# Kernel tuning notes

Measured on AMD Instinct MI355X. Metric: run time of the kernel, lower is better.

The kernel has to match this reference:

```python
import jax, jax.numpy as jnp
import numpy as np

NUM_HEADS = 4

def setup_inputs() -> dict:
    key = jax.random.key(0)
    ks = jax.random.split(key, 9)
    C = 256
    def w(k, shape, scale):
        return jax.random.normal(k, shape, dtype=jnp.float32) * scale
    s = 1.0 / np.sqrt(C)
    return {
        'x':  w(ks[0], (1, C, 48, 48), 1.0),
        'Wq': w(ks[1], (C, C), s), 'bq': w(ks[2], (C,), 0.01),
        'Wk': w(ks[3], (C, C), s), 'bk': w(ks[4], (C,), 0.01),
        'Wv': w(ks[5], (C, C), s), 'bv': w(ks[6], (C,), 0.01),
        'Wo': w(ks[7], (C, C), s), 'bo': w(ks[8], (C,), 0.01),
    }

def reference(x, Wq, bq, Wk, bk, Wv, bv, Wo, bo):
    # x: [B, C, H, W] (NCHW like torch). 1x1 convs == per-pixel matmuls in NHWC.
    B, C, H, W = x.shape
    nh = NUM_HEADS
    xt = jnp.transpose(x, (0, 2, 3, 1))                 # [B,H,W,C]
    q = xt @ Wq.T + bq                                  # [B,H,W,Ck]
    k = xt @ Wk.T + bk                                  # [B,H,W,Ck]
    v = xt @ Wv.T + bv                                  # [B,H,W,Cv]
    dk = q.shape[-1] // nh
    dv = v.shape[-1] // nh
    # split heads then FULLY flatten (batch*H*W*heads), as in the original
    qf = q.reshape(B * H * W * nh, dk) / jnp.sqrt(jnp.float32(dk))
    kf = k.reshape(B * H * W * nh, dk)
    vf = v.reshape(B * H * W * nh, dv)
    A = jax.nn.softmax(qf @ kf.T, axis=1)               # [N,N], N = B*H*W*nh
    # dropout is identity in eval mode
    O = A @ vf                                          # [N,dv]
    O = O.reshape(B, H, W, nh * dv)                     # heads folded back into channels
    out = O @ Wo.T + bo                                 # 1x1 output conv
    return jnp.transpose(out, (0, 3, 1, 2))             # [B,Cout,H,W]
```

## Files before the change

### kernel.cpp

```cpp
#include <hip/hip_runtime.h>
#include <stdint.h>

typedef __attribute__((ext_vector_type(4))) float f32x4;
typedef __attribute__((ext_vector_type(8))) short bf16x8;

#define MFMA(a, b, c) __builtin_amdgcn_mfma_f32_16x16x32_bf16(a, b, c, 0, 0, 0)

__device__ __forceinline__ short f2b(float f) {
    uint32_t u = __builtin_bit_cast(uint32_t, f);
    u += 0x7fffu + ((u >> 16) & 1u);
    return (short)(u >> 16);
}

__device__ __forceinline__ float ex2(float x) {
    float r; asm("v_exp_f32 %0, %1" : "=v"(r) : "v"(x)); return r;
}
__device__ __forceinline__ uint32_t cvtpk(float lo, float hi) {
    uint32_t r; asm("v_cvt_pk_bf16_f32 %0, %1, %2" : "=v"(r) : "v"(lo), "v"(hi)); return r;
}
__device__ __forceinline__ float lo2f(uint32_t u) {
    return __builtin_bit_cast(float, (uint32_t)(u << 16));
}
__device__ __forceinline__ float hi2f(uint32_t u) {
    return __builtin_bit_cast(float, (uint32_t)(u & 0xffff0000u));
}

typedef __attribute__((address_space(1))) const uint32_t gu32;
typedef __attribute__((address_space(3))) uint32_t su32;
__device__ __forceinline__ void stage16(const void* g, void* s) {
    __builtin_amdgcn_global_load_lds((gu32*)g, (su32*)s, 16, 0, 0);
}

__device__ __forceinline__ int FSW(int r) { return (r & 3) | (((r >> 3) & 1) << 2); }

#define QSCALE 0.1803368801111601f

__global__ __launch_bounds__(256) void k_prep(
    const float* __restrict__ x,
    const float* __restrict__ Wq, const float* __restrict__ Wk,
    const float* __restrict__ Wv, const float* __restrict__ Wo,
    short* __restrict__ Wall, short* __restrict__ xt) {
    __shared__ float tile[64][65];
    if (blockIdx.x < 1024) {
        int idx = blockIdx.x * 256 + threadIdx.x;
        int row = idx >> 8, col = idx & 255;
        float v;
        if (row < 256)      v = Wq[row * 256 + col];
        else if (row < 512) v = Wk[(row - 256) * 256 + col];
        else if (row < 768) v = Wv[(row - 512) * 256 + col];
        else                v = Wo[(row - 768) * 256 + col];
        Wall[idx] = f2b(v);
    } else {
        int b = blockIdx.x - 1024;
        int pbase = (b % 36) * 64, cbase = (b / 36) * 64;
        int tx = threadIdx.x & 63, tq = threadIdx.x >> 6;
        #pragma unroll
        for (int r = 0; r < 16; r++) {
            int row = tq * 16 + r;
            tile[row][tx] = x[(cbase + row) * 2304 + pbase + tx];
        }
        __syncthreads();
        #pragma unroll
        for (int r = 0; r < 16; r++) {
            int prow = tq * 16 + r;
            xt[(pbase + prow) * 256 + cbase + tx] = f2b(tile[tx][prow]);
        }
    }
}

__global__ __launch_bounds__(256) void k_gemm_qkv(
    const short* __restrict__ Wall, const short* __restrict__ xt,
    const float* __restrict__ bq, const float* __restrict__ bk, const float* __restrict__ bv,
    short* __restrict__ Qf, short* __restrict__ Kf, short* __restrict__ Vt) {
    int t = threadIdx.x, wave = t >> 6, lane = t & 63, lr = lane & 15, lg = lane >> 4;
    int obase = blockIdx.x * 64 + wave * 16;
    int pbase = blockIdx.y * 64;
    const short* arow  = Wall + (obase + lr) * 256 + lg * 8;
    const short* brow0 = xt + (pbase +  0 + lr) * 256 + lg * 8;
    const short* brow1 = xt + (pbase + 16 + lr) * 256 + lg * 8;
    const short* brow2 = xt + (pbase + 32 + lr) * 256 + lg * 8;
    const short* brow3 = xt + (pbase + 48 + lr) * 256 + lg * 8;
    f32x4 acc0 = {0,0,0,0}, acc1 = {0,0,0,0}, acc2 = {0,0,0,0}, acc3 = {0,0,0,0};
    #pragma unroll
    for (int ks = 0; ks < 8; ks++) {
        bf16x8 a = *(const bf16x8*)(arow + ks * 32);
        acc0 = MFMA(a, *(const bf16x8*)(brow0 + ks * 32), acc0);
        acc1 = MFMA(a, *(const bf16x8*)(brow1 + ks * 32), acc1);
        acc2 = MFMA(a, *(const bf16x8*)(brow2 + ks * 32), acc2);
        acc3 = MFMA(a, *(const bf16x8*)(brow3 + ks * 32), acc3);
    }
    int w_idx = obase >> 8;
    const float* bias = (w_idx == 0) ? bq : (w_idx == 1) ? bk : bv;
    f32x4 accs[4] = {acc0, acc1, acc2, acc3};
    #pragma unroll
    for (int i = 0; i < 4; i++) {
        int o = obase + 4 * lg + i;
        int oo = o & 255;
        float b = bias[oo];
        int h = oo >> 6, d = oo & 63;
        #pragma unroll
        for (int ct = 0; ct < 4; ct++) {
            int p = pbase + ct * 16 + lr;
            float val = accs[ct][i] + b;
            int n = p * 4 + h;
            if (w_idx == 0)      Qf[n * 64 + d] = f2b(val * QSCALE);
            else if (w_idx == 1) Kf[n * 64 + d] = f2b(val);
            else                 Vt[d * 9216 + n] = f2b(val);
        }
    }
}

__global__ __launch_bounds__(256) void k_attn(
    const short* __restrict__ Qf, const short* __restrict__ Kf,
    const short* __restrict__ Vt, int keysPer, int ntiles,
    float* __restrict__ ps, uint32_t* __restrict__ pacc) {
    __shared__ short ktile[2][4096];
    __shared__ short vtile[2][4096];
    int t = threadIdx.x, wave = t >> 6, lane = t & 63, lr = lane & 15, lg = lane >> 4;
    int kb = blockIdx.y;
    int qbase = blockIdx.x * 128 + wave * 16;
    int kstart = kb * keysPer;

    const short* qrowA = Qf + (qbase + lr) * 64 + lg * 8;
    bf16x8 qA0 = *(const bf16x8*)(qrowA);
    bf16x8 qA1 = *(const bf16x8*)(qrowA + 32);
    const short* qrowB = qrowA + 64 * 64;
    bf16x8 qB0 = *(const bf16x8*)(qrowB);
    bf16x8 qB1 = *(const bf16x8*)(qrowB + 32);

    bf16x8 ones;
    #pragma unroll
    for (int i = 0; i < 8; i++) ones[i] = (short)0x3F80;

    int sr = lane >> 3, slot = lane & 7;
    int srow0 = wave * 16 + sr, srow1 = srow0 + 8;
    int col0 = (slot ^ FSW(srow0)) << 4;
    int col1 = (slot ^ FSW(srow1)) << 4;
    const char* kS0 = (const char*)Kf + (size_t)(kstart + srow0) * 128 + col0;
    const char* kS1 = (const char*)Kf + (size_t)(kstart + srow1) * 128 + col1;
    const char* vS0 = (const char*)Vt + (size_t)srow0 * 18432 + (size_t)kstart * 2 + col0;
    const char* vS1 = (const char*)Vt + (size_t)srow1 * 18432 + (size_t)kstart * 2 + col1;
    short* kD0[2] = { &ktile[0][wave * 1024], &ktile[1][wave * 1024] };
    short* kD1[2] = { kD0[0] + 512, kD0[1] + 512 };
    short* vD0[2] = { &vtile[0][wave * 1024], &vtile[1][wave * 1024] };
    short* vD1[2] = { vD0[0] + 512, vD0[1] + 512 };

    int perm = (lr & 3) + 8 * (lr >> 2);
    int cb = lg * 16;
    int kOffA0 = perm * 128       + (cb        ^ (FSW(perm) << 4));
    int kOffA1 = perm * 128       + ((cb + 64) ^ (FSW(perm) << 4));
    int kOffB0 = (perm + 4) * 128 + (cb        ^ (FSW(perm + 4) << 4));
    int kOffB1 = (perm + 4) * 128 + ((cb + 64) ^ (FSW(perm + 4) << 4));
    int vOff   = lr * 128         + (cb        ^ (FSW(lr) << 4));

    f32x4 zv = {0,0,0,0};
    f32x4 accA0 = zv, accA1 = zv, accA2 = zv, accA3 = zv, saccA = zv;
    f32x4 accB0 = zv, accB1 = zv, accB2 = zv, accB3 = zv, saccB = zv;

    stage16(kS0, kD0[0]); stage16(kS1, kD1[0]);
    stage16(vS0, vD0[0]); stage16(vS1, vD1[0]);

    for (int tt = 0; tt < ntiles; tt++) {
        __syncthreads();
        int buf = tt & 1;
        if (tt + 1 < ntiles) {
            size_t ko = (size_t)(tt + 1) * 8192, vo = (size_t)(tt + 1) * 128;
            stage16(kS0 + ko, kD0[buf ^ 1]); stage16(kS1 + ko, kD1[buf ^ 1]);
            stage16(vS0 + vo, vD0[buf ^ 1]); stage16(vS1 + vo, vD1[buf ^ 1]);
        }
        const char* kt = (const char*)&ktile[buf][0];
        const char* vt = (const char*)&vtile[buf][0];

        bf16x8 kA0 = *(const bf16x8*)(kt + kOffA0);
        bf16x8 kA1 = *(const bf16x8*)(kt + kOffA1);
        bf16x8 kB0 = *(const bf16x8*)(kt + kOffB0);
        bf16x8 kB1 = *(const bf16x8*)(kt + kOffB1);
        f32x4 sA0 = MFMA(kA0, qA0, zv); sA0 = MFMA(kA1, qA1, sA0);
        f32x4 sA1 = MFMA(kB0, qA0, zv); sA1 = MFMA(kB1, qA1, sA1);
        f32x4 sB0 = MFMA(kA0, qB0, zv); sB0 = MFMA(kA1, qB1, sB0);
        f32x4 sB1 = MFMA(kB0, qB0, zv); sB1 = MFMA(kB1, qB1, sB1);
        kA0 = *(const bf16x8*)(kt + 4096 + kOffA0);
        kA1 = *(const bf16x8*)(kt + 4096 + kOffA1);
        kB0 = *(const bf16x8*)(kt + 4096 + kOffB0);
        kB1 = *(const bf16x8*)(kt + 4096 + kOffB1);
        f32x4 sA2 = MFMA(kA0, qA0, zv); sA2 = MFMA(kA1, qA1, sA2);
        f32x4 sA3 = MFMA(kB0, qA0, zv); sA3 = MFMA(kB1, qA1, sA3);
        f32x4 sB2 = MFMA(kA0, qB0, zv); sB2 = MFMA(kA1, qB1, sB2);
        f32x4 sB3 = MFMA(kB0, qB0, zv); sB3 = MFMA(kB1, qB1, sB3);

        union { uint32_t w[4]; bf16x8 v; } paA, pbA, paB, pbB;
        paA.w[0] = cvtpk(ex2(sA0[0]), ex2(sA0[1]));
        paA.w[1] = cvtpk(ex2(sA0[2]), ex2(sA0[3]));
        paA.w[2] = cvtpk(ex2(sA1[0]), ex2(sA1[1]));
        paA.w[3] = cvtpk(ex2(sA1[2]), ex2(sA1[3]));
        pbA.w[0] = cvtpk(ex2(sA2[0]), ex2(sA2[1]));
        pbA.w[1] = cvtpk(ex2(sA2[2]), ex2(sA2[3]));
        pbA.w[2] = cvtpk(ex2(sA3[0]), ex2(sA3[1]));
        pbA.w[3] = cvtpk(ex2(sA3[2]), ex2(sA3[3]));
        paB.w[0] = cvtpk(ex2(sB0[0]), ex2(sB0[1]));
        paB.w[1] = cvtpk(ex2(sB0[2]), ex2(sB0[3]));
        paB.w[2] = cvtpk(ex2(sB1[0]), ex2(sB1[1]));
        paB.w[3] = cvtpk(ex2(sB1[2]), ex2(sB1[3]));
        pbB.w[0] = cvtpk(ex2(sB2[0]), ex2(sB2[1]));
        pbB.w[1] = cvtpk(ex2(sB2[2]), ex2(sB2[3]));
        pbB.w[2] = cvtpk(ex2(sB3[0]), ex2(sB3[1]));
        pbB.w[3] = cvtpk(ex2(sB3[2]), ex2(sB3[3]));

        bf16x8 v0a = *(const bf16x8*)(vt + vOff);
        bf16x8 v0b = *(const bf16x8*)(vt + (vOff ^ 64));
        bf16x8 v1a = *(const bf16x8*)(vt + vOff + 2048);
        bf16x8 v1b = *(const bf16x8*)(vt + ((vOff + 2048) ^ 64));
        bf16x8 v2a = *(const bf16x8*)(vt + vOff + 4096);
        bf16x8 v2b = *(const bf16x8*)(vt + ((vOff + 4096) ^ 64));
        bf16x8 v3a = *(const bf16x8*)(vt + vOff + 6144);
        bf16x8 v3b = *(const bf16x8*)(vt + ((vOff + 6144) ^ 64));
        accA0 = MFMA(v0a, paA.v, accA0); accA0 = MFMA(v0b, pbA.v, accA0);
        accA1 = MFMA(v1a, paA.v, accA1); accA1 = MFMA(v1b, pbA.v, accA1);
        accA2 = MFMA(v2a, paA.v, accA2); accA2 = MFMA(v2b, pbA.v, accA2);
        accA3 = MFMA(v3a, paA.v, accA3); accA3 = MFMA(v3b, pbA.v, accA3);
        saccA = MFMA(ones, paA.v, saccA); saccA = MFMA(ones, pbA.v, saccA);
        accB0 = MFMA(v0a, paB.v, accB0); accB0 = MFMA(v0b, pbB.v, accB0);
        accB1 = MFMA(v1a, paB.v, accB1); accB1 = MFMA(v1b, pbB.v, accB1);
        accB2 = MFMA(v2a, paB.v, accB2); accB2 = MFMA(v2b, pbB.v, accB2);
        accB3 = MFMA(v3a, paB.v, accB3); accB3 = MFMA(v3b, pbB.v, accB3);
        saccB = MFMA(ones, paB.v, saccB); saccB = MFMA(ones, pbB.v, saccB);
    }

    int gA = blockIdx.x * 8 + wave;
    int gB = gA + 4;
    int pidxA = kb * 576 + gA, pidxB = kb * 576 + gB;
    uint2* outA = (uint2*)pacc + (size_t)pidxA * 256 + lr * 16 + lg;
    uint2* outB = (uint2*)pacc + (size_t)pidxB * 256 + lr * 16 + lg;
    uint2 w;
    w.x = cvtpk(accA0[0], accA0[1]); w.y = cvtpk(accA0[2], accA0[3]); outA[0]  = w;
    w.x = cvtpk(accA1[0], accA1[1]); w.y = cvtpk(accA1[2], accA1[3]); outA[4]  = w;
    w.x = cvtpk(accA2[0], accA2[1]); w.y = cvtpk(accA2[2], accA2[3]); outA[8]  = w;
    w.x = cvtpk(accA3[0], accA3[1]); w.y = cvtpk(accA3[2], accA3[3]); outA[12] = w;
    w.x = cvtpk(accB0[0], accB0[1]); w.y = cvtpk(accB0[2], accB0[3]); outB[0]  = w;
    w.x = cvtpk(accB1[0], accB1[1]); w.y = cvtpk(accB1[2], accB1[3]); outB[4]  = w;
    w.x = cvtpk(accB2[0], accB2[1]); w.y = cvtpk(accB2[2], accB2[3]); outB[8]  = w;
    w.x = cvtpk(accB3[0], accB3[1]); w.y = cvtpk(accB3[2], accB3[3]); outB[12] = w;
    if (lg == 0) {
        ps[pidxA * 16 + lr] = saccA[0];
        ps[pidxB * 16 + lr] = saccB[0];
    }
}

__global__ __launch_bounds__(256) void k_attn_combine(
    const float* __restrict__ ps, const uint32_t* __restrict__ pacc,
    short* __restrict__ Of, int nsplit) {
    int qb = blockIdx.x, t = threadIdx.x;
    int q = t >> 4, dv4 = (t & 15) * 4;
    float S = 0.f;
    f32x4 O = {0, 0, 0, 0};
    for (int s = 0; s < nsplit; s++) {
        S += ps[(s * 576 + qb) * 16 + q];
        uint2 v = ((const uint2*)pacc)[(size_t)(s * 576 + qb) * 256 + t];
        O[0] += lo2f(v.x); O[1] += hi2f(v.x);
        O[2] += lo2f(v.y); O[3] += hi2f(v.y);
    }
    float inv = 1.0f / S;
    uint32_t w0 = cvtpk(O[0] * inv, O[1] * inv);
    uint32_t w1 = cvtpk(O[2] * inv, O[3] * inv);
    int n = qb * 16 + q, p = n >> 2, hh = n & 3;
    uint2 pk; pk.x = w0; pk.y = w1;
    *(uint2*)(&Of[p * 256 + hh * 64 + dv4]) = pk;
}

__global__ __launch_bounds__(256) void k_gemm_out(
    const short* __restrict__ Wo_bf, const short* __restrict__ Of,
    const float* __restrict__ bo, float* __restrict__ out) {
    int t = threadIdx.x, wave = t >> 6, lane = t & 63, lr = lane & 15, lg = lane >> 4;
    int obase = blockIdx.x * 64 + wave * 16;
    int pbase = blockIdx.y * 64;
    const short* arow  = Wo_bf + (obase + lr) * 256 + lg * 8;
    const short* brow0 = Of + (pbase +  0 + lr) * 256 + lg * 8;
    const short* brow1 = Of + (pbase + 16 + lr) * 256 + lg * 8;
    const short* brow2 = Of + (pbase + 32 + lr) * 256 + lg * 8;
    const short* brow3 = Of + (pbase + 48 + lr) * 256 + lg * 8;
    f32x4 acc0 = {0,0,0,0}, acc1 = {0,0,0,0}, acc2 = {0,0,0,0}, acc3 = {0,0,0,0};
    #pragma unroll
    for (int ks = 0; ks < 8; ks++) {
        bf16x8 a = *(const bf16x8*)(arow + ks * 32);
        acc0 = MFMA(a, *(const bf16x8*)(brow0 + ks * 32), acc0);
        acc1 = MFMA(a, *(const bf16x8*)(brow1 + ks * 32), acc1);
        acc2 = MFMA(a, *(const bf16x8*)(brow2 + ks * 32), acc2);
        acc3 = MFMA(a, *(const bf16x8*)(brow3 + ks * 32), acc3);
    }
    f32x4 accs[4] = {acc0, acc1, acc2, acc3};
    #pragma unroll
    for (int i = 0; i < 4; i++) {
        int o = obase + 4 * lg + i;
        float b = bo[o];
        #pragma unroll
        for (int ct = 0; ct < 4; ct++) {
            int p = pbase + ct * 16 + lr;
            out[o * 2304 + p] = accs[ct][i] + b;
        }
    }
}

extern "C" void kernel_launch(void* const* d_in, const int* in_sizes, int n_in,
                              void* d_out, int out_size, void* d_ws, size_t ws_size,
                              hipStream_t stream) {
    const float* x  = (const float*)d_in[0];
    const float* Wq = (const float*)d_in[1];
    const float* bq = (const float*)d_in[2];
    const float* Wk = (const float*)d_in[3];
    const float* bk = (const float*)d_in[4];
    const float* Wv = (const float*)d_in[5];
    const float* bv = (const float*)d_in[6];
    const float* Wo = (const float*)d_in[7];
    const float* bo = (const float*)d_in[8];

    char* ws = (char*)d_ws;
    short* Wall = (short*)(ws);
    short* xt   = (short*)(ws + 524288);
    short* Qf   = (short*)(ws + 1703936);
    short* Kf   = (short*)(ws + 2883584);
    short* Vt   = (short*)(ws + 4063232);
    short* Of   = (short*)(ws + 5242880);
    float* ps   = (float*)(ws + 6422528);
    uint32_t* pacc = (uint32_t*)(ws + 7012352);
    float* out  = (float*)d_out;

    int nsplit = (ws_size >= (size_t)7012352 + 16u * 576u * 2048u) ? 16 : 8;
    int keysPer = 9216 / nsplit;
    int ntiles = keysPer / 64;

    k_prep<<<1168, 256, 0, stream>>>(x, Wq, Wk, Wv, Wo, Wall, xt);
    k_gemm_qkv<<<dim3(12, 36), 256, 0, stream>>>(Wall, xt, bq, bk, bv, Qf, Kf, Vt);
    k_attn<<<dim3(72, nsplit), 256, 0, stream>>>(Qf, Kf, Vt, keysPer, ntiles, ps, pacc);
    k_attn_combine<<<576, 256, 0, stream>>>(ps, pacc, Of, nsplit);
    k_gemm_out<<<dim3(4, 36), 256, 0, stream>>>(Wall + 768 * 256, Of, bo, out);
}
```

Baseline: 68.37 us.

## Fuse split-K combine into output projection and add MFMA priority hints

The attention-combine kernel and the output 1x1-conv GEMM are merged into one kernel. Each block reduces the split partial sums for 16 pixels into a shared-memory tile and immediately multiplies it by Wo, so the Of intermediate never goes to global memory and one launch is dropped. s_setprio is also raised around the MFMA clusters in the attention loop so those waves get issue priority. The fused kernel launches only 144 blocks and each block reloads all of Wo, which trades away parallelism and load reuse.

```diff
diff --git a/kernel.cpp b/kernel.cpp
--- a/kernel.cpp
+++ b/kernel.cpp
@@ -175,18 +175,22 @@
         bf16x8 kA1 = *(const bf16x8*)(kt + kOffA1);
         bf16x8 kB0 = *(const bf16x8*)(kt + kOffB0);
         bf16x8 kB1 = *(const bf16x8*)(kt + kOffB1);
+        __builtin_amdgcn_s_setprio(1);
         f32x4 sA0 = MFMA(kA0, qA0, zv); sA0 = MFMA(kA1, qA1, sA0);
         f32x4 sA1 = MFMA(kB0, qA0, zv); sA1 = MFMA(kB1, qA1, sA1);
         f32x4 sB0 = MFMA(kA0, qB0, zv); sB0 = MFMA(kA1, qB1, sB0);
         f32x4 sB1 = MFMA(kB0, qB0, zv); sB1 = MFMA(kB1, qB1, sB1);
+        __builtin_amdgcn_s_setprio(0);
         kA0 = *(const bf16x8*)(kt + 4096 + kOffA0);
         kA1 = *(const bf16x8*)(kt + 4096 + kOffA1);
         kB0 = *(const bf16x8*)(kt + 4096 + kOffB0);
         kB1 = *(const bf16x8*)(kt + 4096 + kOffB1);
+        __builtin_amdgcn_s_setprio(1);
         f32x4 sA2 = MFMA(kA0, qA0, zv); sA2 = MFMA(kA1, qA1, sA2);
         f32x4 sA3 = MFMA(kB0, qA0, zv); sA3 = MFMA(kB1, qA1, sA3);
         f32x4 sB2 = MFMA(kA0, qB0, zv); sB2 = MFMA(kA1, qB1, sB2);
         f32x4 sB3 = MFMA(kB0, qB0, zv); sB3 = MFMA(kB1, qB1, sB3);
+        __builtin_amdgcn_s_setprio(0);
 
         union { uint32_t w[4]; bf16x8 v; } paA, pbA, paB, pbB;
         paA.w[0] = cvtpk(ex2(sA0[0]), ex2(sA0[1]));
@@ -214,6 +218,7 @@
         bf16x8 v2b = *(const bf16x8*)(vt + ((vOff + 4096) ^ 64));
         bf16x8 v3a = *(const bf16x8*)(vt + vOff + 6144);
         bf16x8 v3b = *(const bf16x8*)(vt + ((vOff + 6144) ^ 64));
+        __builtin_amdgcn_s_setprio(1);
         accA0 = MFMA(v0a, paA.v, accA0); accA0 = MFMA(v0b, pbA.v, accA0);
         accA1 = MFMA(v1a, paA.v, accA1); accA1 = MFMA(v1b, pbA.v, accA1);
         accA2 = MFMA(v2a, paA.v, accA2); accA2 = MFMA(v2b, pbA.v, accA2);
@@ -224,6 +229,7 @@
         accB2 = MFMA(v2a, paB.v, accB2); accB2 = MFMA(v2b, pbB.v, accB2);
         accB3 = MFMA(v3a, paB.v, accB3); accB3 = MFMA(v3b, pbB.v, accB3);
         saccB = MFMA(ones, paB.v, saccB); saccB = MFMA(ones, pbB.v, saccB);
+        __builtin_amdgcn_s_setprio(0);
     }
 
     int gA = blockIdx.x * 8 + wave;
@@ -246,56 +252,54 @@
     }
 }
 
-__global__ __launch_bounds__(256) void k_attn_combine(
+__global__ __launch_bounds__(256) void k_out(
     const float* __restrict__ ps, const uint32_t* __restrict__ pacc,
-    short* __restrict__ Of, int nsplit) {
-    int qb = blockIdx.x, t = threadIdx.x;
+    const short* __restrict__ Wo_bf, const float* __restrict__ bo,
+    float* __restrict__ out, int nsplit) {
+    __shared__ short Bt[16 * 264];
+    int t = threadIdx.x;
+    int b = blockIdx.x;
     int q = t >> 4, dv4 = (t & 15) * 4;
-    float S = 0.f;
-    f32x4 O = {0, 0, 0, 0};
-    for (int s = 0; s < nsplit; s++) {
-        S += ps[(s * 576 + qb) * 16 + q];
-        uint2 v = ((const uint2*)pacc)[(size_t)(s * 576 + qb) * 256 + t];
-        O[0] += lo2f(v.x); O[1] += hi2f(v.x);
-        O[2] += lo2f(v.y); O[3] += hi2f(v.y);
-    }
-    float inv = 1.0f / S;
-    uint32_t w0 = cvtpk(O[0] * inv, O[1] * inv);
-    uint32_t w1 = cvtpk(O[2] * inv, O[3] * inv);
-    int n = qb * 16 + q, p = n >> 2, hh = n & 3;
-    uint2 pk; pk.x = w0; pk.y = w1;
-    *(uint2*)(&Of[p * 256 + hh * 64 + dv4]) = pk;
-}
-
-__global__ __launch_bounds__(256) void k_gemm_out(
-    const short* __restrict__ Wo_bf, const short* __restrict__ Of,
-    const float* __restrict__ bo, float* __restrict__ out) {
-    int t = threadIdx.x, wave = t >> 6, lane = t & 63, lr = lane & 15, lg = lane >> 4;
-    int obase = blockIdx.x * 64 + wave * 16;
-    int pbase = blockIdx.y * 64;
-    const short* arow  = Wo_bf + (obase + lr) * 256 + lg * 8;
-    const short* brow0 = Of + (pbase +  0 + lr) * 256 + lg * 8;
-    const short* brow1 = Of + (pbase + 16 + lr) * 256 + lg * 8;
-    const short* brow2 = Of + (pbase + 32 + lr) * 256 + lg * 8;
-    const short* brow3 = Of + (pbase + 48 + lr) * 256 + lg * 8;
+    #pragma unroll
+    for (int ql = 0; ql < 4; ql++) {
+        int qb = b * 4 + ql;
+        float S = 0.f;
+        f32x4 O = {0, 0, 0, 0};
+        for (int s = 0; s < nsplit; s++) {
+            S += ps[(s * 576 + qb) * 16 + q];
+            uint2 v = ((const uint2*)pacc)[(size_t)(s * 576 + qb) * 256 + t];
+            O[0] += lo2f(v.x); O[1] += hi2f(v.x);
+            O[2] += lo2f(v.y); O[3] += hi2f(v.y);
+        }
+        float inv = 1.0f / S;
+        uint2 pk;
+        pk.x = cvtpk(O[0] * inv, O[1] * inv);
+        pk.y = cvtpk(O[2] * inv, O[3] * inv);
+        int nl = ql * 16 + q;
+        int pl = nl >> 2, c = (nl & 3) * 64 + dv4;
+        *(uint2*)(&Bt[pl * 264 + c]) = pk;
+    }
+    __syncthreads();
+    int wave = t >> 6, lane = t & 63, lr = lane & 15, lg = lane >> 4;
+    const short* arow = Wo_bf + (wave * 64 + lr) * 256 + lg * 8;
+    const short* brow = &Bt[lr * 264 + lg * 8];
     f32x4 acc0 = {0,0,0,0}, acc1 = {0,0,0,0}, acc2 = {0,0,0,0}, acc3 = {0,0,0,0};
     #pragma unroll
     for (int ks = 0; ks < 8; ks++) {
-        bf16x8 a = *(const bf16x8*)(arow + ks * 32);
-        acc0 = MFMA(a, *(const bf16x8*)(brow0 + ks * 32), acc0);
-        acc1 = MFMA(a, *(const bf16x8*)(brow1 + ks * 32), acc1);
-        acc2 = MFMA(a, *(const bf16x8*)(brow2 + ks * 32), acc2);
-        acc3 = MFMA(a, *(const bf16x8*)(brow3 + ks * 32), acc3);
+        bf16x8 bf = *(const bf16x8*)(brow + ks * 32);
+        acc0 = MFMA(*(const bf16x8*)(arow +    0 + ks * 32), bf, acc0);
+        acc1 = MFMA(*(const bf16x8*)(arow + 4096 + ks * 32), bf, acc1);
+        acc2 = MFMA(*(const bf16x8*)(arow + 8192 + ks * 32), bf, acc2);
+        acc3 = MFMA(*(const bf16x8*)(arow + 12288 + ks * 32), bf, acc3);
     }
     f32x4 accs[4] = {acc0, acc1, acc2, acc3};
-    #pragma unroll
-    for (int i = 0; i < 4; i++) {
-        int o = obase + 4 * lg + i;
-        float b = bo[o];
+    int pg = b * 16 + lr;
+    #pragma unroll
+    for (int j = 0; j < 4; j++) {
         #pragma unroll
-        for (int ct = 0; ct < 4; ct++) {
-            int p = pbase + ct * 16 + lr;
-            out[o * 2304 + p] = accs[ct][i] + b;
+        for (int i = 0; i < 4; i++) {
+            int o = wave * 64 + j * 16 + 4 * lg + i;
+            out[o * 2304 + pg] = accs[j][i] + bo[o];
         }
     }
 }
@@ -319,7 +323,6 @@
     short* Qf   = (short*)(ws + 1703936);
     short* Kf   = (short*)(ws + 2883584);
     short* Vt   = (short*)(ws + 4063232);
-    short* Of   = (short*)(ws + 5242880);
     float* ps   = (float*)(ws + 6422528);
     uint32_t* pacc = (uint32_t*)(ws + 7012352);
     float* out  = (float*)d_out;
@@ -331,6 +334,5 @@
     k_prep<<<1168, 256, 0, stream>>>(x, Wq, Wk, Wv, Wo, Wall, xt);
     k_gemm_qkv<<<dim3(12, 36), 256, 0, stream>>>(Wall, xt, bq, bk, bv, Qf, Kf, Vt);
     k_attn<<<dim3(72, nsplit), 256, 0, stream>>>(Qf, Kf, Vt, keysPer, ntiles, ps, pacc);
-    k_attn_combine<<<576, 256, 0, stream>>>(ps, pacc, Of, nsplit);
-    k_gemm_out<<<dim3(4, 36), 256, 0, stream>>>(Wall + 768 * 256, Of, bo, out);
-}
+    k_out<<<144, 256, 0, stream>>>(ps, pacc, Wall + 768 * 256, bo, out, nsplit);
+}
```

After: 81.14 us. 18.7% more time.
